# Optimization experiments

Measured on AMD Instinct MI355X. Metric: run time of the kernel, lower is better.

## Reference

```python
import jax, jax.numpy as jnp
import numpy as np

# tcnn HashGrid config from ntc_conf
L = 16            # n_levels
T = 1 << 15       # 2**log2_hashmap_size entries per level
F = 4             # n_features_per_level
BASE = 16.0       # base_resolution
N_PTS = 1_000_000
PRIMES = jnp.array([1, 2654435761, 805459861], dtype=jnp.uint32)  # tcnn spatial hash primes
OFFS = np.array([[(c >> 2) & 1, (c >> 1) & 1, c & 1] for c in range(8)], dtype=np.uint32)  # 8 cube corners


def hash_encode(x, table):
    """Multi-resolution hash grid encoding. x: [N,3] in [0,1], table: [L,T,F] -> [N, L*F]."""
    N = x.shape[0]
    scales = BASE * (2.0 ** jnp.arange(L, dtype=jnp.float32))        # [L]
    pos = x[:, None, :] * scales[None, :, None]                      # [N,L,3]
    p0 = jnp.floor(pos)
    frac = pos - p0                                                  # trilinear weights source
    p0u = p0.astype(jnp.uint32)
    flat_table = table.reshape(L * T, F)
    level_off = (jnp.arange(L, dtype=jnp.uint32) * jnp.uint32(T))[None, :]  # [1,L]
    acc = jnp.zeros((N, L, F), dtype=table.dtype)
    for c in range(8):  # fixed 8 corners -> keeps peak memory at [N,L,F] per corner
        off = jnp.asarray(OFFS[c])                                   # [3] uint32
        corner = p0u + off                                           # [N,L,3]
        h = corner * PRIMES                                          # uint32 wraparound mul
        idx = (h[..., 0] ^ h[..., 1] ^ h[..., 2]) & jnp.uint32(T - 1)  # [N,L]
        feats = flat_table[(idx + level_off).astype(jnp.int32)]      # gather [N,L,F]
        w = jnp.prod(jnp.where(off.astype(bool), frac, 1.0 - frac), axis=-1)  # [N,L]
        acc = acc + w[..., None] * feats
    return acc.reshape(N, L * F)


def setup_inputs() -> dict:
    key = jax.random.key(0)
    k1, k2, k3, k4, k5 = jax.random.split(key, 5)
    xyz = jax.random.normal(k1, (N_PTS, 3), dtype=jnp.float32)
    xyz_bound_min = -jnp.ones((3,), dtype=jnp.float32)
    xyz_bound_max = jnp.ones((3,), dtype=jnp.float32)
    hash_table = jax.random.normal(k2, (L, T, F), dtype=jnp.float32) * 1e-2  # tcnn-style small init
    w0 = jax.random.normal(k3, (64, 64), dtype=jnp.float32) * (1.0 / 8.0)
    w1 = jax.random.normal(k4, (64, 64), dtype=jnp.float32) * (1.0 / 8.0)
    w2 = jax.random.normal(k5, (64, 8), dtype=jnp.float32) * (1.0 / 8.0)
    return {"xyz": xyz, "xyz_bound_min": xyz_bound_min, "xyz_bound_max": xyz_bound_max,
            "hash_table": hash_table, "w0": w0, "w1": w1, "w2": w2}


def reference(xyz, xyz_bound_min, xyz_bound_max, hash_table, w0, w1, w2):
    contracted = (xyz - xyz_bound_min) / (xyz_bound_max - xyz_bound_min)   # [N,3]
    mask = jnp.all((contracted >= 0.0) & (contracted <= 1.0), axis=1)      # [N]
    # Evaluate on all points (clamped) and mask the writes -- equivalent to the
    # original compaction (contracted[mask]) + scatter-back, jit-friendly shapes.
    xin = jnp.clip(contracted, 0.0, 1.0)
    enc = hash_encode(xin, hash_table)                                     # [N,64]
    h = jax.nn.relu(enc @ w0)
    h = jax.nn.relu(h @ w1)
    resi = h @ w2                                                          # [N,8]
    d_xyz = jnp.where(mask[:, None], resi[:, :3], 0.0)
    ident_rot = jnp.array([1.0, 0.0, 0.0, 0.0], dtype=resi.dtype)
    d_rot = jnp.where(mask[:, None], resi[:, 3:7], ident_rot)
    return mask, d_xyz, d_rot
```

## Files before the change

### kernel.cpp

```cpp
#include <hip/hip_runtime.h>
#include <hip/hip_bf16.h>


#define LVL 16
#define TSZ 32768
#define PR1 2654435761u
#define PR2 805459861u

typedef __attribute__((ext_vector_type(8))) short bf16x8;
typedef __attribute__((ext_vector_type(4))) float f32x4;
typedef __attribute__((ext_vector_type(2))) float f32x2;
typedef __attribute__((ext_vector_type(4))) unsigned short u16x4;
typedef __attribute__((ext_vector_type(2))) unsigned int u32x2;
typedef long long i64;

__device__ __forceinline__ unsigned short f2bf(float f) {
    return __builtin_bit_cast(unsigned short, __float2bfloat16(f));
}

__device__ __forceinline__ unsigned f32x4_to_fp8x4(float f0, float f1, float f2, float f3) {
#if __has_builtin(__builtin_amdgcn_cvt_pk_fp8_f32)
    int u = 0;
    u = __builtin_amdgcn_cvt_pk_fp8_f32(f0, f1, u, false);
    u = __builtin_amdgcn_cvt_pk_fp8_f32(f2, f3, u, true);
    return (unsigned)u;
#else
    float ff[4] = { f0, f1, f2, f3 };
    unsigned u = 0;
    for (int k = 0; k < 4; ++k) {
        const float v = ff[k];
        const unsigned s = v < 0.f ? 1u : 0u;
        float av = fabsf(v);
        unsigned b;
        if (av < 6.103515625e-05f) {
            b = 0u;
        } else if (av < 0.015625f) {
            b = (unsigned)rintf(av * 512.f);
        } else {
            int e; float m = frexpf(av, &e);
            unsigned E = (unsigned)(e - 1 + 7);
            unsigned q = (unsigned)rintf(m * 16.f);
            if (q == 16u) { q = 8u; ++E; }
            b = (E << 3) | (q - 8u);
        }
        u |= ((s << 7) | b) << (8 * k);
    }
    return u;
#endif
}

__device__ __forceinline__ unsigned char f32_to_fp8(float v) {
    return (unsigned char)(f32x4_to_fp8x4(v, v, v, v) & 0xffu);
}

__device__ __forceinline__ void fp8x4_to_f32(unsigned r, float f[4]) {
#if __has_builtin(__builtin_amdgcn_cvt_pk_f32_fp8)
    const f32x2 lo = __builtin_amdgcn_cvt_pk_f32_fp8((int)r, false);
    const f32x2 hi = __builtin_amdgcn_cvt_pk_f32_fp8((int)r, true);
    f[0] = lo[0]; f[1] = lo[1]; f[2] = hi[0]; f[3] = hi[1];
#else
#pragma unroll
    for (int k = 0; k < 4; ++k) {
        const unsigned b = (r >> (8 * k)) & 0xffu;
        const unsigned s = b >> 7, em = b & 0x7fu, e = em >> 3, m = em & 7u;
        float v;
        if (e) v = __builtin_bit_cast(float, ((e + 120u) << 23) | (m << 20));
        else   v = (float)m * 0.001953125f;
        f[k] = s ? -v : v;
    }
#endif
}

__global__ __launch_bounds__(256) void k_tbl8(
    const float* __restrict__ t, unsigned* __restrict__ o, int n4,
    const float* __restrict__ w0, const float* __restrict__ w1,
    const float* __restrict__ w2, char* __restrict__ wbase)
{
    const int g = blockIdx.x * 256 + threadIdx.x;
    if (g < n4) {
        const float4 a = reinterpret_cast<const float4*>(t)[g];
        o[g] = f32x4_to_fp8x4(a.x * 256.f, a.y * 256.f, a.z * 256.f, a.w * 256.f);
    }
    if (blockIdx.x == gridDim.x - 1) {
        const int tt = threadIdx.x;
        unsigned char*  wf8 = (unsigned char*)wbase;
        unsigned short* wf1 = (unsigned short*)(wbase + 4096);
        unsigned short* wf2 = (unsigned short*)(wbase + 4096 + 8192);
#pragma unroll
        for (int q = 0; q < 16; ++q) {
            const int s = q * 256 + tt;
            const int e = s & 7, f = s >> 3;
            const int ln = f & 63, ntkk = f >> 6;
            const int k = (ntkk & 1) * 32 + (ln >> 4) * 8 + e;
            const int n = (ntkk >> 1) * 16 + (ln & 15);
            wf8[s] = f32_to_fp8(w0[k * 64 + n]);
        }
#pragma unroll
        for (int q = 0; q < 16; ++q) {
            const int s = q * 256 + tt;
            const int e = s & 7, f = s >> 3;
            const int ln = f & 63, ntkk = f >> 6;
            const int k = (ntkk & 1) * 32 + (ln >> 4) * 8 + e;
            const int n = (ntkk >> 1) * 16 + (ln & 15);
            wf1[s] = f2bf(w1[k * 64 + n]);
        }
#pragma unroll
        for (int q = 0; q < 4; ++q) {
            const int s = q * 256 + tt;
            const int e = s & 7, f = s >> 3;
            const int ln = f & 63, kk = f >> 6;
            const int k = kk * 32 + (ln >> 4) * 8 + e;
            const int n = ln & 15;
            wf2[s] = (n < 8) ? f2bf(w2[k * 8 + n]) : (unsigned short)0;
        }
    }
}

__global__ __launch_bounds__(1024) void k_enc(
    const float* __restrict__ xyz, const float* __restrict__ bmin, const float* __restrict__ bmax,
    const unsigned* __restrict__ tbl8, float* __restrict__ out,
    unsigned* __restrict__ enc, int N, int Npad)
{
    __shared__ unsigned tabL[TSZ];

    const int t = threadIdx.x;
    const int base = blockIdx.x * 4096;

    const float bx0 = bmin[0], by0 = bmin[1], bz0 = bmin[2];
    const float ex = bmax[0] - bx0, ey = bmax[1] - by0, ez = bmax[2] - bz0;

    float X[4], Y[4], Z[4];
#pragma unroll
    for (int q = 0; q < 4; ++q) {
        const int p  = base + q * 1024 + t;
        const int pc = p < N ? p : N - 1;
        const float cx = (xyz[3 * pc + 0] - bx0) / ex;
        const float cy = (xyz[3 * pc + 1] - by0) / ey;
        const float cz = (xyz[3 * pc + 2] - bz0) / ez;
        const bool inside = (cx >= 0.f) && (cx <= 1.f) && (cy >= 0.f) && (cy <= 1.f) &&
                            (cz >= 0.f) && (cz <= 1.f);
        if (p < N) out[p] = inside ? 1.f : 0.f;
        X[q] = fminf(fmaxf(cx, 0.f), 1.f);
        Y[q] = fminf(fmaxf(cy, 0.f), 1.f);
        Z[q] = fminf(fmaxf(cz, 0.f), 1.f);
    }

    unsigned pend[4];

    for (int l = 0; l < LVL; ++l) {
        __syncthreads();
        {
            const uint4* __restrict__ src = reinterpret_cast<const uint4*>(tbl8 + (size_t)l * TSZ);
            uint4* dst = reinterpret_cast<uint4*>(tabL);
#pragma unroll
            for (int j = 0; j < 8; ++j) dst[j * 1024 + t] = src[j * 1024 + t];
        }
        __syncthreads();

        const float scale = 16.f * (float)(1u << l);
#pragma unroll
        for (int q = 0; q < 4; ++q) {
            const float px = X[q] * scale, py = Y[q] * scale, pz = Z[q] * scale;
            const float fx = floorf(px), fy = floorf(py), fz = floorf(pz);
            const float rx = px - fx, ry = py - fy, rz = pz - fz;
            const unsigned ux = (unsigned)fx, uy = (unsigned)fy, uz = (unsigned)fz;
            const unsigned hx[2] = { ux, ux + 1u };
            const unsigned hy[2] = { uy * PR1, uy * PR1 + PR1 };
            const unsigned hz[2] = { uz * PR2, uz * PR2 + PR2 };
            const float wx0 = 1.f - rx, wx1 = rx;
            const float wy0 = 1.f - ry, wy1 = ry;
            const float wz[2] = { 1.f - rz, rz };
            const float wxy[4] = { wx0 * wy0, wx0 * wy1, wx1 * wy0, wx1 * wy1 };

            unsigned r[8];
#pragma unroll
            for (int c = 0; c < 8; ++c)
                r[c] = tabL[(hx[(c >> 2) & 1] ^ hy[(c >> 1) & 1] ^ hz[c & 1]) & (TSZ - 1u)];

            float a0 = 0.f, a1 = 0.f, a2 = 0.f, a3 = 0.f;
#pragma unroll
            for (int c = 0; c < 8; ++c) {
                float f[4];
                fp8x4_to_f32(r[c], f);
                const float w = wxy[c >> 1] * wz[c & 1];
                a0 = fmaf(w, f[0], a0);
                a1 = fmaf(w, f[1], a1);
                a2 = fmaf(w, f[2], a2);
                a3 = fmaf(w, f[3], a3);
            }

            const unsigned v = f32x4_to_fp8x4(a0, a1, a2, a3);
            if (l & 1) {
                const int p = base + q * 1024 + t;
                const u32x2 v2 = { pend[q], v };
                __builtin_nontemporal_store(v2,
                    reinterpret_cast<u32x2*>(enc) + ((size_t)(l >> 1) * Npad + p));
            } else {
                pend[q] = v;
            }
        }
    }
}

__global__ __launch_bounds__(256) void k_mlp(
    const char* __restrict__ wbase, const unsigned* __restrict__ enc,
    float* __restrict__ out, int N, int Npad)
{
    __shared__ unsigned short hT[8 * 256 * 8];
    __shared__ float resS[256 * 8];

    const unsigned char*  wf8 = (const unsigned char*)wbase;
    const unsigned short* wf1 = (const unsigned short*)(wbase + 4096);
    const unsigned short* wf2 = (const unsigned short*)(wbase + 4096 + 8192);

    const int t = threadIdx.x, wv = t >> 6, ln = t & 63;
    const int col = ln & 15, g = ln >> 4;
    const int ptb = blockIdx.x * 256;
    const int i = ptb + t;

    u32x2 a0[2][4];
#pragma unroll
    for (int kk = 0; kk < 2; ++kk)
#pragma unroll
        for (int mt = 0; mt < 4; ++mt) {
            const size_t pt = (size_t)ptb + wv * 64 + mt * 16 + col;
            a0[kk][mt] = __builtin_nontemporal_load(
                reinterpret_cast<const u32x2*>(enc) + ((size_t)(kk * 4 + g) * Npad + pt));
        }
    u32x2 b0[4][2];
#pragma unroll
    for (int nt = 0; nt < 4; ++nt)
#pragma unroll
        for (int kk = 0; kk < 2; ++kk)
            b0[nt][kk] = *reinterpret_cast<const u32x2*>(wf8 + ((nt * 2 + kk) * 64 + ln) * 8);

    f32x4 acc[4][4];
#pragma unroll
    for (int mt = 0; mt < 4; ++mt)
#pragma unroll
        for (int nt = 0; nt < 4; ++nt) acc[mt][nt] = (f32x4){0.f, 0.f, 0.f, 0.f};

#pragma unroll
    for (int kk = 0; kk < 2; ++kk)
#pragma unroll
        for (int nt = 0; nt < 4; ++nt)
#pragma unroll
            for (int mt = 0; mt < 4; ++mt)
                acc[mt][nt] = __builtin_amdgcn_mfma_f32_16x16x32_fp8_fp8(
                    __builtin_bit_cast(i64, a0[kk][mt]),
                    __builtin_bit_cast(i64, b0[nt][kk]), acc[mt][nt], 0, 0, 0);

#pragma unroll
    for (int mt = 0; mt < 4; ++mt)
#pragma unroll
        for (int nt = 0; nt < 4; ++nt) {
            const int kt = nt * 2 + (col >> 3), j = col & 7;
#pragma unroll
            for (int r = 0; r < 4; ++r)
                hT[kt * 2048 + (wv * 64 + mt * 16 + g * 4 + r) * 8 + j] =
                    f2bf(fmaxf(acc[mt][nt][r], 0.f) * 0.00390625f);
        }

    bf16x8 b1[4][2];
#pragma unroll
    for (int nt = 0; nt < 4; ++nt)
#pragma unroll
        for (int kk = 0; kk < 2; ++kk)
            b1[nt][kk] = *reinterpret_cast<const bf16x8*>(wf1 + ((nt * 2 + kk) * 64 + ln) * 8);

#pragma unroll
    for (int mt = 0; mt < 4; ++mt)
#pragma unroll
        for (int nt = 0; nt < 4; ++nt) acc[mt][nt] = (f32x4){0.f, 0.f, 0.f, 0.f};

#pragma unroll
    for (int kk = 0; kk < 2; ++kk) {
        bf16x8 a[4];
#pragma unroll
        for (int mt = 0; mt < 4; ++mt)
            a[mt] = *reinterpret_cast<bf16x8*>(
                &hT[(kk * 4 + g) * 2048 + (wv * 64 + mt * 16 + col) * 8]);
#pragma unroll
        for (int nt = 0; nt < 4; ++nt)
#pragma unroll
            for (int mt = 0; mt < 4; ++mt)
                acc[mt][nt] = __builtin_amdgcn_mfma_f32_16x16x32_bf16(a[mt], b1[nt][kk], acc[mt][nt], 0, 0, 0);
    }

#pragma unroll
    for (int mt = 0; mt < 4; ++mt)
#pragma unroll
        for (int nt = 0; nt < 4; ++nt) {
            const int kt = nt * 2 + (col >> 3), j = col & 7;
#pragma unroll
            for (int r = 0; r < 4; ++r)
                hT[kt * 2048 + (wv * 64 + mt * 16 + g * 4 + r) * 8 + j] =
                    f2bf(fmaxf(acc[mt][nt][r], 0.f));
        }

    f32x4 acc2[4];
#pragma unroll
    for (int mt = 0; mt < 4; ++mt) acc2[mt] = (f32x4){0.f, 0.f, 0.f, 0.f};

#pragma unroll
    for (int kk = 0; kk < 2; ++kk) {
        const bf16x8 b2 = *reinterpret_cast<const bf16x8*>(wf2 + (kk * 64 + ln) * 8);
        bf16x8 a[4];
#pragma unroll
        for (int mt = 0; mt < 4; ++mt)
            a[mt] = *reinterpret_cast<bf16x8*>(
                &hT[(kk * 4 + g) * 2048 + (wv * 64 + mt * 16 + col) * 8]);
#pragma unroll
        for (int mt = 0; mt < 4; ++mt)
            acc2[mt] = __builtin_amdgcn_mfma_f32_16x16x32_bf16(a[mt], b2, acc2[mt], 0, 0, 0);
    }

    if (col < 8) {
#pragma unroll
        for (int mt = 0; mt < 4; ++mt)
#pragma unroll
            for (int r = 0; r < 4; ++r)
                resS[(wv * 64 + mt * 16 + g * 4 + r) * 8 + col] = acc2[mt][r];
    }
    __syncthreads();

    if (i < N) {
        const bool inside = (out[i] != 0.f);
        const f32x4 lo = *reinterpret_cast<f32x4*>(&resS[t * 8 + 0]);
        const f32x4 hi = *reinterpret_cast<f32x4*>(&resS[t * 8 + 4]);

        float* __restrict__ dxyz = out + N;
        dxyz[3 * i + 0] = inside ? lo.x : 0.f;
        dxyz[3 * i + 1] = inside ? lo.y : 0.f;
        dxyz[3 * i + 2] = inside ? lo.z : 0.f;

        float4* __restrict__ drot = reinterpret_cast<float4*>(out + 4 * (size_t)N);
        drot[i] = inside ? make_float4(lo.w, hi.x, hi.y, hi.z)
                         : make_float4(1.f, 0.f, 0.f, 0.f);
    }
}

__global__ __launch_bounds__(256) void ntc_fused(
    const float* __restrict__ xyz, const float* __restrict__ bmin, const float* __restrict__ bmax,
    const float* __restrict__ table, const float* __restrict__ w0, const float* __restrict__ w1,
    const float* __restrict__ w2, float* __restrict__ out, int N)
{
    __shared__ unsigned short encT[8 * 256 * 8];
    __shared__ unsigned short w0t[64 * 64];
    __shared__ unsigned short w1t[64 * 64];
    __shared__ unsigned short w2t[16 * 64];

    const int t = threadIdx.x, wv = t >> 6, ln = t & 63;
    const int col = ln & 15, g = ln >> 4;

#pragma unroll
    for (int it = 0; it < 16; ++it) {
        const int idx = it * 256 + t;
        const int k = idx >> 6, n = idx & 63;
        w0t[n * 64 + k] = f2bf(w0[idx]);
        w1t[n * 64 + k] = f2bf(w1[idx]);
    }
#pragma unroll
    for (int q = 0; q < 4; ++q) {
        const int idx = t * 4 + q;
        const int n = idx >> 6, k = idx & 63;
        w2t[idx] = (n < 8) ? f2bf(w2[k * 8 + n]) : (unsigned short)0;
    }

    const int i = blockIdx.x * 256 + t;
    const int ic = (i < N) ? i : (N - 1);
    const float bx0 = bmin[0], by0 = bmin[1], bz0 = bmin[2];
    const float ex = bmax[0] - bx0, ey = bmax[1] - by0, ez = bmax[2] - bz0;
    const float cx = (xyz[3 * ic + 0] - bx0) / ex;
    const float cy = (xyz[3 * ic + 1] - by0) / ey;
    const float cz = (xyz[3 * ic + 2] - bz0) / ez;
    const bool inside = (cx >= 0.f) && (cx <= 1.f) && (cy >= 0.f) && (cy <= 1.f) &&
                        (cz >= 0.f) && (cz <= 1.f);
    const float x = fminf(fmaxf(cx, 0.f), 1.f);
    const float y = fminf(fmaxf(cy, 0.f), 1.f);
    const float z = fminf(fmaxf(cz, 0.f), 1.f);
    const float4* __restrict__ tab = reinterpret_cast<const float4*>(table);

    for (int l = 0; l < LVL; ++l) {
        const float scale = 16.f * (float)(1u << l);
        const float px = x * scale, py = y * scale, pz = z * scale;
        const float fx = floorf(px), fy = floorf(py), fz = floorf(pz);
        const float rx = px - fx, ry = py - fy, rz = pz - fz;
        const unsigned ux = (unsigned)fx, uy = (unsigned)fy, uz = (unsigned)fz;
        const unsigned hx[2] = { ux, ux + 1u };
        const unsigned hy[2] = { uy * PR1, (uy + 1u) * PR1 };
        const unsigned hz[2] = { uz * PR2, (uz + 1u) * PR2 };
        const float wx[2] = { 1.f - rx, rx };
        const float wy[2] = { 1.f - ry, ry };
        const float wz[2] = { 1.f - rz, rz };
        float a0 = 0.f, a1 = 0.f, a2 = 0.f, a3 = 0.f;
#pragma unroll
        for (int c = 0; c < 8; ++c) {
            const int ox = (c >> 2) & 1, oy = (c >> 1) & 1, oz = c & 1;
            const unsigned idx = (hx[ox] ^ hy[oy] ^ hz[oz]) & (TSZ - 1u);
            const float4 f4 = tab[l * TSZ + idx];
            const float w = wx[ox] * wy[oy] * wz[oz];
            a0 = fmaf(w, f4.x, a0); a1 = fmaf(w, f4.y, a1);
            a2 = fmaf(w, f4.z, a2); a3 = fmaf(w, f4.w, a3);
        }
        u16x4 v = { f2bf(a0), f2bf(a1), f2bf(a2), f2bf(a3) };
        *reinterpret_cast<u16x4*>(&encT[(l >> 1) * 2048 + t * 8 + (l & 1) * 4]) = v;
    }
    __syncthreads();

    f32x4 acc[4][4];
#pragma unroll
    for (int mt = 0; mt < 4; ++mt)
#pragma unroll
        for (int nt = 0; nt < 4; ++nt) acc[mt][nt] = (f32x4){0.f, 0.f, 0.f, 0.f};
#pragma unroll
    for (int kk = 0; kk < 2; ++kk) {
        bf16x8 a[4];
#pragma unroll
        for (int mt = 0; mt < 4; ++mt)
            a[mt] = *reinterpret_cast<bf16x8*>(&encT[(kk * 4 + g) * 2048 + (wv * 64 + mt * 16 + col) * 8]);
#pragma unroll
        for (int nt = 0; nt < 4; ++nt) {
            bf16x8 b = *reinterpret_cast<bf16x8*>(&w0t[(nt * 16 + col) * 64 + kk * 32 + g * 8]);
#pragma unroll
            for (int mt = 0; mt < 4; ++mt)
                acc[mt][nt] = __builtin_amdgcn_mfma_f32_16x16x32_bf16(a[mt], b, acc[mt][nt], 0, 0, 0);
        }
    }
    __syncthreads();
#pragma unroll
    for (int mt = 0; mt < 4; ++mt)
#pragma unroll
        for (int nt = 0; nt < 4; ++nt) {
            const int kt = nt * 2 + (col >> 3), j = col & 7;
#pragma unroll
            for (int r = 0; r < 4; ++r)
                encT[kt * 2048 + (wv * 64 + mt * 16 + g * 4 + r) * 8 + j] = f2bf(fmaxf(acc[mt][nt][r], 0.f));
        }
    __syncthreads();
#pragma unroll
    for (int mt = 0; mt < 4; ++mt)
#pragma unroll
        for (int nt = 0; nt < 4; ++nt) acc[mt][nt] = (f32x4){0.f, 0.f, 0.f, 0.f};
#pragma unroll
    for (int kk = 0; kk < 2; ++kk) {
        bf16x8 a[4];
#pragma unroll
        for (int mt = 0; mt < 4; ++mt)
            a[mt] = *reinterpret_cast<bf16x8*>(&encT[(kk * 4 + g) * 2048 + (wv * 64 + mt * 16 + col) * 8]);
#pragma unroll
        for (int nt = 0; nt < 4; ++nt) {
            bf16x8 b = *reinterpret_cast<bf16x8*>(&w1t[(nt * 16 + col) * 64 + kk * 32 + g * 8]);
#pragma unroll
            for (int mt = 0; mt < 4; ++mt)
                acc[mt][nt] = __builtin_amdgcn_mfma_f32_16x16x32_bf16(a[mt], b, acc[mt][nt], 0, 0, 0);
        }
    }
    __syncthreads();
#pragma unroll
    for (int mt = 0; mt < 4; ++mt)
#pragma unroll
        for (int nt = 0; nt < 4; ++nt) {
            const int kt = nt * 2 + (col >> 3), j = col & 7;
#pragma unroll
            for (int r = 0; r < 4; ++r)
                encT[kt * 2048 + (wv * 64 + mt * 16 + g * 4 + r) * 8 + j] = f2bf(fmaxf(acc[mt][nt][r], 0.f));
        }
    __syncthreads();
    f32x4 acc2[4];
#pragma unroll
    for (int mt = 0; mt < 4; ++mt) acc2[mt] = (f32x4){0.f, 0.f, 0.f, 0.f};
#pragma unroll
    for (int kk = 0; kk < 2; ++kk) {
        bf16x8 a[4];
#pragma unroll
        for (int mt = 0; mt < 4; ++mt)
            a[mt] = *reinterpret_cast<bf16x8*>(&encT[(kk * 4 + g) * 2048 + (wv * 64 + mt * 16 + col) * 8]);
        bf16x8 b = *reinterpret_cast<bf16x8*>(&w2t[col * 64 + kk * 32 + g * 8]);
#pragma unroll
        for (int mt = 0; mt < 4; ++mt)
            acc2[mt] = __builtin_amdgcn_mfma_f32_16x16x32_bf16(a[mt], b, acc2[mt], 0, 0, 0);
    }
    __syncthreads();
    float* res = reinterpret_cast<float*>(encT);
    if (col < 8) {
#pragma unroll
        for (int mt = 0; mt < 4; ++mt)
#pragma unroll
            for (int r = 0; r < 4; ++r)
                res[(wv * 64 + mt * 16 + g * 4 + r) * 8 + col] = acc2[mt][r];
    }
    __syncthreads();
    if (i < N) {
        const f32x4 lo = *reinterpret_cast<f32x4*>(&res[t * 8 + 0]);
        const f32x4 hi = *reinterpret_cast<f32x4*>(&res[t * 8 + 4]);
        out[i] = inside ? 1.f : 0.f;
        float* __restrict__ dxyz = out + N;
        dxyz[3 * i + 0] = inside ? lo.x : 0.f;
        dxyz[3 * i + 1] = inside ? lo.y : 0.f;
        dxyz[3 * i + 2] = inside ? lo.z : 0.f;
        float4* __restrict__ drot = reinterpret_cast<float4*>(out + 4 * (size_t)N);
        drot[i] = inside ? make_float4(lo.w, hi.x, hi.y, hi.z)
                         : make_float4(1.f, 0.f, 0.f, 0.f);
    }
}

extern "C" void kernel_launch(void* const* d_in, const int* in_sizes, int n_in,
                              void* d_out, int out_size, void* d_ws, size_t ws_size,
                              hipStream_t stream) {
    const float* xyz   = (const float*)d_in[0];
    const float* bmin  = (const float*)d_in[1];
    const float* bmax  = (const float*)d_in[2];
    const float* table = (const float*)d_in[3];
    const float* w0    = (const float*)d_in[4];
    const float* w1    = (const float*)d_in[5];
    const float* w2    = (const float*)d_in[6];
    float* out = (float*)d_out;

    const int N = in_sizes[0] / 3;
    const int nb = (N + 255) / 256;
    const int nbE = (N + 4095) / 4096;
    const int Npad = nbE * 4096;
    const int tblElems = in_sizes[3];

    size_t offW = ((size_t)tblElems + 63) & ~(size_t)63;
    size_t offEnc = (offW + 14336 + 255) & ~(size_t)255;
    size_t need = offEnc + (size_t)Npad * 64;

    if (ws_size >= need) {
        unsigned* tbl8 = (unsigned*)d_ws;
        char* wbase    = (char*)d_ws + offW;
        unsigned* enc  = (unsigned*)((char*)d_ws + offEnc);
        const int n4 = tblElems / 4;
        k_tbl8<<<(n4 + 255) / 256, 256, 0, stream>>>(table, tbl8, n4, w0, w1, w2, wbase);
        k_enc<<<nbE, 1024, 0, stream>>>(xyz, bmin, bmax, tbl8, out, enc, N, Npad);
        k_mlp<<<nb, 256, 0, stream>>>(wbase, enc, out, N, Npad);
    } else {
        ntc_fused<<<nb, 256, 0, stream>>>(xyz, bmin, bmax, table, w0, w1, w2, out, N);
    }
}
```

Before: 191.1 us.

## Make encoder blocks level-persistent so each block loads one level table once

The encoder grid becomes 16 levels × 32 sub-blocks. Each block loads a single level's fp8 table into LDS once and then grid-strides over all points, instead of reloading 16 tables per 4096-point chunk. This removes the repeated table copies and the barriers between levels. The cost is that every block re-reads xyz and recomputes the contraction, and the next point's coordinates are prefetched to hide that. Encodings are now stored per level as 4-byte values, so k_mlp gathers two separate loads per pair. The hash index is also pre-shifted into a byte offset, and accumulation uses packed f32x2 math.

```diff
diff --git a/kernel.cpp b/kernel.cpp
--- a/kernel.cpp
+++ b/kernel.cpp
@@ -6,6 +6,8 @@
 #define TSZ 32768
 #define PR1 2654435761u
 #define PR2 805459861u
+#define SUBS 32
+#define STRIDE (SUBS * 1024)
 
 typedef __attribute__((ext_vector_type(8))) short bf16x8;
 typedef __attribute__((ext_vector_type(4))) float f32x4;
@@ -53,12 +55,12 @@
     return (unsigned char)(f32x4_to_fp8x4(v, v, v, v) & 0xffu);
 }
 
-__device__ __forceinline__ void fp8x4_to_f32(unsigned r, float f[4]) {
+__device__ __forceinline__ void fp8x4_to_2f32x2(unsigned r, f32x2& lo, f32x2& hi) {
 #if __has_builtin(__builtin_amdgcn_cvt_pk_f32_fp8)
-    const f32x2 lo = __builtin_amdgcn_cvt_pk_f32_fp8((int)r, false);
-    const f32x2 hi = __builtin_amdgcn_cvt_pk_f32_fp8((int)r, true);
-    f[0] = lo[0]; f[1] = lo[1]; f[2] = hi[0]; f[3] = hi[1];
+    lo = __builtin_amdgcn_cvt_pk_f32_fp8((int)r, false);
+    hi = __builtin_amdgcn_cvt_pk_f32_fp8((int)r, true);
 #else
+    float f[4];
 #pragma unroll
     for (int k = 0; k < 4; ++k) {
         const unsigned b = (r >> (8 * k)) & 0xffu;
@@ -68,6 +70,8 @@
         else   v = (float)m * 0.001953125f;
         f[k] = s ? -v : v;
     }
+    lo = (f32x2){ f[0], f[1] };
+    hi = (f32x2){ f[2], f[3] };
 #endif
 }
 
@@ -123,81 +127,90 @@
 {
     __shared__ unsigned tabL[TSZ];
 
-    const int t = threadIdx.x;
-    const int base = blockIdx.x * 4096;
+    const int t   = threadIdx.x;
+    const int l   = blockIdx.x & 15;
+    const int sub = blockIdx.x >> 4;
+
+    {
+        const uint4* __restrict__ src = reinterpret_cast<const uint4*>(tbl8 + (size_t)l * TSZ);
+        uint4* dst = reinterpret_cast<uint4*>(tabL);
+#pragma unroll
+        for (int j = 0; j < 8; ++j) dst[j * 1024 + t] = src[j * 1024 + t];
+    }
+    __syncthreads();
 
     const float bx0 = bmin[0], by0 = bmin[1], bz0 = bmin[2];
-    const float ex = bmax[0] - bx0, ey = bmax[1] - by0, ez = bmax[2] - bz0;
-
-    float X[4], Y[4], Z[4];
-#pragma unroll
-    for (int q = 0; q < 4; ++q) {
-        const int p  = base + q * 1024 + t;
-        const int pc = p < N ? p : N - 1;
-        const float cx = (xyz[3 * pc + 0] - bx0) / ex;
-        const float cy = (xyz[3 * pc + 1] - by0) / ey;
-        const float cz = (xyz[3 * pc + 2] - bz0) / ez;
-        const bool inside = (cx >= 0.f) && (cx <= 1.f) && (cy >= 0.f) && (cy <= 1.f) &&
-                            (cz >= 0.f) && (cz <= 1.f);
-        if (p < N) out[p] = inside ? 1.f : 0.f;
-        X[q] = fminf(fmaxf(cx, 0.f), 1.f);
-        Y[q] = fminf(fmaxf(cy, 0.f), 1.f);
-        Z[q] = fminf(fmaxf(cz, 0.f), 1.f);
-    }
-
-    unsigned pend[4];
-
-    for (int l = 0; l < LVL; ++l) {
-        __syncthreads();
-        {
-            const uint4* __restrict__ src = reinterpret_cast<const uint4*>(tbl8 + (size_t)l * TSZ);
-            uint4* dst = reinterpret_cast<uint4*>(tabL);
-#pragma unroll
-            for (int j = 0; j < 8; ++j) dst[j * 1024 + t] = src[j * 1024 + t];
-        }
-        __syncthreads();
-
-        const float scale = 16.f * (float)(1u << l);
-#pragma unroll
-        for (int q = 0; q < 4; ++q) {
-            const float px = X[q] * scale, py = Y[q] * scale, pz = Z[q] * scale;
+    const float iex = 1.f / (bmax[0] - bx0);
+    const float iey = 1.f / (bmax[1] - by0);
+    const float iez = 1.f / (bmax[2] - bz0);
+    const float scale = 16.f * (float)(1u << l);
+    unsigned* __restrict__ encL = enc + (size_t)l * Npad;
+    const bool isL0 = (l == 0);
+
+    int p = sub * 1024 + t;
+    if (p < Npad) {
+        int pc = p < N ? p : N - 1;
+        float cxr = xyz[3 * pc + 0], cyr = xyz[3 * pc + 1], czr = xyz[3 * pc + 2];
+
+        for (; p < Npad; ) {
+            const int pn  = p + STRIDE;
+            const int pnc = pn < N ? pn : N - 1;
+            const float nxr = xyz[3 * pnc + 0];
+            const float nyr = xyz[3 * pnc + 1];
+            const float nzr = xyz[3 * pnc + 2];
+
+            const float ccx = (cxr - bx0) * iex;
+            const float ccy = (cyr - by0) * iey;
+            const float ccz = (czr - bz0) * iez;
+            if (isL0 && p < N) {
+                const bool inside = (ccx >= 0.f) && (ccx <= 1.f) && (ccy >= 0.f) &&
+                                    (ccy <= 1.f) && (ccz >= 0.f) && (ccz <= 1.f);
+                out[p] = inside ? 1.f : 0.f;
+            }
+            const float x = fminf(fmaxf(ccx, 0.f), 1.f);
+            const float y = fminf(fmaxf(ccy, 0.f), 1.f);
+            const float z = fminf(fmaxf(ccz, 0.f), 1.f);
+
+            const float px = x * scale, py = y * scale, pz = z * scale;
             const float fx = floorf(px), fy = floorf(py), fz = floorf(pz);
             const float rx = px - fx, ry = py - fy, rz = pz - fz;
             const unsigned ux = (unsigned)fx, uy = (unsigned)fy, uz = (unsigned)fz;
-            const unsigned hx[2] = { ux, ux + 1u };
-            const unsigned hy[2] = { uy * PR1, uy * PR1 + PR1 };
-            const unsigned hz[2] = { uz * PR2, uz * PR2 + PR2 };
-            const float wx0 = 1.f - rx, wx1 = rx;
-            const float wy0 = 1.f - ry, wy1 = ry;
-            const float wz[2] = { 1.f - rz, rz };
-            const float wxy[4] = { wx0 * wy0, wx0 * wy1, wx1 * wy0, wx1 * wy1 };
+
+            const unsigned hy0 = uy * PR1, hz0 = uz * PR2;
+            const unsigned M2 = (TSZ - 1u) << 2;
+            const unsigned hxy2[4] = {
+                ((ux        ^ hy0)         << 2) & M2,
+                ((ux        ^ (hy0 + PR1)) << 2) & M2,
+                (((ux + 1u) ^ hy0)         << 2) & M2,
+                (((ux + 1u) ^ (hy0 + PR1)) << 2) & M2 };
+            const unsigned hz2[2] = { (hz0 << 2) & M2, ((hz0 + PR2) << 2) & M2 };
+
+            const float wx0 = 1.f - rx, wy0 = 1.f - ry;
+            const float wz0 = 1.f - rz;
+            const float wxy[4] = { wx0 * wy0, wx0 * ry, rx * wy0, rx * ry };
+            const float wzz[2] = { wz0, rz };
 
             unsigned r[8];
 #pragma unroll
             for (int c = 0; c < 8; ++c)
-                r[c] = tabL[(hx[(c >> 2) & 1] ^ hy[(c >> 1) & 1] ^ hz[c & 1]) & (TSZ - 1u)];
-
-            float a0 = 0.f, a1 = 0.f, a2 = 0.f, a3 = 0.f;
+                r[c] = *reinterpret_cast<const unsigned*>(
+                    reinterpret_cast<const char*>(tabL) + (hxy2[c >> 1] ^ hz2[c & 1]));
+
+            f32x2 a01 = { 0.f, 0.f }, a23 = { 0.f, 0.f };
 #pragma unroll
             for (int c = 0; c < 8; ++c) {
-                float f[4];
-                fp8x4_to_f32(r[c], f);
-                const float w = wxy[c >> 1] * wz[c & 1];
-                a0 = fmaf(w, f[0], a0);
-                a1 = fmaf(w, f[1], a1);
-                a2 = fmaf(w, f[2], a2);
-                a3 = fmaf(w, f[3], a3);
+                f32x2 lo, hi;
+                fp8x4_to_2f32x2(r[c], lo, hi);
+                const float w = wxy[c >> 1] * wzz[c & 1];
+                const f32x2 w2 = { w, w };
+                a01 += w2 * lo;
+                a23 += w2 * hi;
             }
 
-            const unsigned v = f32x4_to_fp8x4(a0, a1, a2, a3);
-            if (l & 1) {
-                const int p = base + q * 1024 + t;
-                const u32x2 v2 = { pend[q], v };
-                __builtin_nontemporal_store(v2,
-                    reinterpret_cast<u32x2*>(enc) + ((size_t)(l >> 1) * Npad + p));
-            } else {
-                pend[q] = v;
-            }
+            const unsigned v = f32x4_to_fp8x4(a01[0], a01[1], a23[0], a23[1]);
+            __builtin_nontemporal_store(v, encL + p);
+
+            p = pn; cxr = nxr; cyr = nyr; czr = nzr;
         }
     }
 }
@@ -224,8 +237,11 @@
 #pragma unroll
         for (int mt = 0; mt < 4; ++mt) {
             const size_t pt = (size_t)ptb + wv * 64 + mt * 16 + col;
-            a0[kk][mt] = __builtin_nontemporal_load(
-                reinterpret_cast<const u32x2*>(enc) + ((size_t)(kk * 4 + g) * Npad + pt));
+            const int j = kk * 4 + g;
+            u32x2 a;
+            a[0] = __builtin_nontemporal_load(enc + (size_t)(2 * j)     * Npad + pt);
+            a[1] = __builtin_nontemporal_load(enc + (size_t)(2 * j + 1) * Npad + pt);
+            a0[kk][mt] = a;
         }
     u32x2 b0[4][2];
 #pragma unroll
@@ -519,8 +535,7 @@
 
     const int N = in_sizes[0] / 3;
     const int nb = (N + 255) / 256;
-    const int nbE = (N + 4095) / 4096;
-    const int Npad = nbE * 4096;
+    const int Npad = ((N + 4095) / 4096) * 4096;
     const int tblElems = in_sizes[3];
 
     size_t offW = ((size_t)tblElems + 63) & ~(size_t)63;
@@ -533,7 +548,7 @@
         unsigned* enc  = (unsigned*)((char*)d_ws + offEnc);
         const int n4 = tblElems / 4;
         k_tbl8<<<(n4 + 255) / 256, 256, 0, stream>>>(table, tbl8, n4, w0, w1, w2, wbase);
-        k_enc<<<nbE, 1024, 0, stream>>>(xyz, bmin, bmax, tbl8, out, enc, N, Npad);
+        k_enc<<<16 * SUBS, 1024, 0, stream>>>(xyz, bmin, bmax, tbl8, out, enc, N, Npad);
         k_mlp<<<nb, 256, 0, stream>>>(wbase, enc, out, N, Npad);
     } else {
         ntc_fused<<<nb, 256, 0, stream>>>(xyz, bmin, bmax, table, w0, w1, w2, out, N);
```

New measurement: 183.3 us. 4.1% less time.
